# Kernel tuning notes

Measured on AMD Instinct MI355X. Metric: run time of the kernel, lower is better.

## Reference

```python
import jax, jax.numpy as jnp
import numpy as np
from jax.scipy.special import logsumexp

K, D, H, A = 8, 512, 512, 1024
S, T = 64, 128
B = S * T


def setup_inputs() -> dict:
    key = jax.random.key(0)
    k1, k2, k3, k4 = jax.random.split(key, 4)
    obs = jax.random.normal(k1, (B, D), dtype=jnp.float32)
    actions = jax.random.randint(k2, (B,), 0, A, dtype=jnp.int64)
    # uniform mixture prior (log(1/K)) => all components supported
    start_mixture_logprobs = jnp.full((S, K), jnp.log(1.0 / K), dtype=jnp.float32)
    W1 = jax.random.normal(k3, (K, D, H), dtype=jnp.float32) * 0.02
    b1 = jnp.zeros((K, H), dtype=jnp.float32)
    W2 = jax.random.normal(k4, (K, H, A), dtype=jnp.float32) * 0.02
    b2 = jnp.zeros((K, A), dtype=jnp.float32)
    return {"obs": obs, "actions": actions,
            "start_mixture_logprobs": start_mixture_logprobs,
            "W1": W1, "b1": b1, "W2": W2, "b2": b2, "seq_len": T}


def reference(obs, actions, start_mixture_logprobs, W1, b1, W2, b2, seq_len):
    num_seqs, num_comp = start_mixture_logprobs.shape
    batch = obs.shape[0]
    t_len = batch // num_seqs  # == seq_len
    num_out = W2.shape[-1]

    # per-component MLP on the full batch (all components supported)
    h = jax.nn.relu(jnp.einsum('bd,kdh->kbh', obs, W1) + b1[:, None, :])
    logits = jnp.einsum('kbh,kha->kba', h, W2) + b2[:, None, :]  # [K,B,A]
    component_logprobs = jax.nn.log_softmax(logits, axis=2)      # [K,B,A]

    # add time dimension: [B, K, A] -> [S, T, K, A]
    clp_t = component_logprobs.transpose(1, 0, 2).reshape(num_seqs, t_len, num_comp, num_out)
    act_t = actions.reshape(num_seqs, t_len)

    # gather logprob of taken action per component: [S, T, K]
    idx = jnp.broadcast_to(act_t[:, :, None, None], (num_seqs, t_len, num_comp, 1))
    action_logprobs = jnp.take_along_axis(clp_t, idx, axis=3)[..., 0]
    cum = jnp.cumsum(action_logprobs, axis=1)  # [S,T,K]

    # per-timestep posterior over mixture (shifted cumulative evidence)
    shift = jnp.concatenate([jnp.zeros((num_seqs, 1, num_comp), dtype=cum.dtype), cum[:, :-1]], axis=1)
    mix = jax.nn.log_softmax(start_mixture_logprobs[:, None, :] + shift, axis=2)  # [S,T,K]
    final_mixture_logprobs = jax.nn.log_softmax(start_mixture_logprobs + cum[:, -1], axis=1)

    # combine: logsumexp over components of component_logprobs + mixture logprob
    mix_flat = mix.reshape(batch, num_comp).T  # [K,B]
    model_out = logsumexp(component_logprobs + mix_flat[:, :, None], axis=0)  # [B,A]
    return model_out, final_mixture_logprobs
```

## Files before the change

kernel.cpp:

```cpp
#include <hip/hip_runtime.h>
#include <hip/hip_bf16.h>
#include <stdint.h>

#define KC   8
#define DIM  512
#define HID  512
#define ACTN 1024
#define NS   64
#define NT   128
#define NB   8192
#define PB   4

typedef __attribute__((ext_vector_type(8))) short short8;
typedef __attribute__((ext_vector_type(8))) unsigned short ushort8;
typedef __attribute__((ext_vector_type(4))) float floatx4;
typedef __attribute__((ext_vector_type(2))) float floatx2;
typedef __attribute__((ext_vector_type(4))) unsigned int uint4v;

__device__ inline float bf2f(unsigned short u) {
    return __uint_as_float(((unsigned int)u) << 16);
}
__device__ inline unsigned short f2bf_rne(float x) {
    unsigned int u = __float_as_uint(x);
    u += 0x7fffu + ((u >> 16) & 1u);
    return (unsigned short)(u >> 16);
}

__device__ inline unsigned char f2fp8_manual(float v) {
    unsigned int s = (__float_as_uint(v) >> 24) & 0x80u;
    float a = fabsf(v) * 0x1.0p-120f;
    unsigned int b = __float_as_uint(a);
    b += 0x7FFFFu + ((b >> 20) & 1u);
    unsigned int m = b >> 20;
    if (m > 0x7Eu) m = 0x7Eu;
    return (unsigned char)(s | m);
}
__device__ inline float fp82f_manual(unsigned int byte) {
    unsigned int bits = ((byte & 0x80u) << 24) | ((byte & 0x7Fu) << 20);
    return __uint_as_float(bits) * 0x1.0p+120f;
}
template <bool HI>
__device__ inline unsigned int pk_fp8(float a, float b, unsigned int old) {
#if __has_builtin(__builtin_amdgcn_cvt_pk_fp8_f32)
    return __builtin_amdgcn_cvt_pk_fp8_f32(a, b, old, HI);
#else
    unsigned int p = (unsigned int)f2fp8_manual(a) | ((unsigned int)f2fp8_manual(b) << 8);
    return HI ? ((old & 0x0000ffffu) | (p << 16)) : ((old & 0xffff0000u) | p);
#endif
}
template <bool HI>
__device__ inline floatx2 unpk_fp8(unsigned int src) {
#if __has_builtin(__builtin_amdgcn_cvt_pk_f32_fp8)
    return __builtin_amdgcn_cvt_pk_f32_fp8(src, HI);
#else
    unsigned int w = HI ? (src >> 16) : src;
    floatx2 r;
    r.x = fp82f_manual(w & 0xffu);
    r.y = fp82f_manual((w >> 8) & 0xffu);
    return r;
#endif
}

__device__ inline void gload_lds16(const unsigned short* g, unsigned short* l) {
    __builtin_amdgcn_global_load_lds(
        (const __attribute__((address_space(1))) unsigned int*)g,
        (__attribute__((address_space(3))) unsigned int*)l,
        16, 0, 0);
}


__global__ __launch_bounds__(256) void prep_kernel(
    const float* __restrict__ obs, const float* __restrict__ W1,
    const float* __restrict__ W2,
    unsigned short* __restrict__ obs_bk, unsigned short* __restrict__ W1bk,
    unsigned short* __restrict__ W2bk)
{
    __shared__ float tile[64][65];
    int id = blockIdx.x;
    if (id < 128) {
        int mg = id;
#pragma unroll
        for (int rep = 0; rep < 16; ++rep) {
            int idx = rep * 256 + threadIdx.x;
            int row = mg * 64 + (idx >> 6);
            int c_all = idx & 63;
            int kt = c_all >> 3, c = c_all & 7;
            const float* p = obs + (size_t)row * DIM + c_all * 8;
            ushort8 u;
#pragma unroll
            for (int e = 0; e < 8; e++) u[e] = f2bf_rne(p[e]);
            size_t off = (((size_t)(row >> 8) * (DIM >> 6) + kt) << 14)
                       + ((size_t)(row & 255) << 6) + ((c ^ (row & 7)) << 3);
            *(ushort8*)(obs_bk + off) = u;
        }
        return;
    }
    const float* src; unsigned short* dst; int R, C, xt, yt;
    if (id < 640) {
        int t = id - 128; int z = t >> 6; int rem = t & 63;
        xt = rem & 7; yt = rem >> 3;
        R = DIM; C = HID;
        src = W1 + (size_t)z * DIM * HID; dst = W1bk + (size_t)z * DIM * HID;
    } else {
        int t = id - 640; int z = t >> 7; int rem = t & 127;
        xt = rem & 15; yt = rem >> 4;
        R = HID; C = ACTN;
        src = W2 + (size_t)z * HID * ACTN; dst = W2bk + (size_t)z * HID * ACTN;
    }
    int h0 = xt * 64, d0 = yt * 64;
    int tx = threadIdx.x & 63, ty = threadIdx.x >> 6;
#pragma unroll
    for (int i = 0; i < 64; i += 4)
        tile[ty + i][tx] = src[(size_t)(d0 + ty + i) * C + h0 + tx];
    __syncthreads();
#pragma unroll
    for (int rep = 0; rep < 2; ++rep) {
        int idx  = rep * 256 + threadIdx.x;
        int h_l  = idx & 63;
        int dc   = idx >> 6;
        int rh   = h0 + h_l;
        ushort8 u;
#pragma unroll
        for (int e = 0; e < 8; e++) u[e] = f2bf_rne(tile[dc * 8 + e][h_l]);
        size_t off = (((size_t)(rh >> 8) * (R >> 6) + (d0 >> 6)) << 14)
                   + ((size_t)(rh & 255) << 6) + ((dc ^ (rh & 7)) << 3);
        *(ushort8*)(dst + off) = u;
    }
}

__global__ __launch_bounds__(512, 2) void gemm_blk_kernel(
    const unsigned short* __restrict__ Aall,
    const unsigned short* __restrict__ Ball,
    const float* __restrict__ biasall,
    void* __restrict__ Call,
    const int* __restrict__ actions,
    float* __restrict__ psum, float* __restrict__ palp,
    int M, int N, int Kd,
    long long zsA, long long zsB,
    int strideBias, long long strideCbytes,
    int do_relu, int do_blocked)
{
    __shared__ __align__(16) unsigned short S[65536];

    const int zb = blockIdx.z;
    const float* bias = biasall + (size_t)zb * strideBias;
    char* const Cbase = (char*)Call + (size_t)zb * strideCbytes;

    const int tid  = threadIdx.x;
    const int lane = tid & 63;
    const int w    = tid >> 6;
    const int wm   = w >> 2;
    const int wn   = w & 3;
    const int quad = lane >> 4;
    const int l16  = lane & 15;

    const int bm = blockIdx.x * 256;
    const int bn = blockIdx.y * 256;
    const int KT = Kd >> 6;
    const int nk = KT;

    floatx4 acc[8][4];
#pragma unroll
    for (int i = 0; i < 8; i++)
#pragma unroll
        for (int j = 0; j < 4; j++)
            acc[i][j] = (floatx4){0.f, 0.f, 0.f, 0.f};

    const unsigned short* srcA = Aall + (size_t)zb * zsA
        + (((size_t)(bm >> 8) * KT) << 14) + w * 1024 + lane * 8;
    const unsigned short* srcB = Ball + (size_t)zb * zsB
        + (((size_t)(bn >> 8) * KT) << 14) + w * 1024 + lane * 8;

    auto stageA = [&](int U, int HF) {
        const unsigned short* g = srcA + U * 16384 + HF * 8192;
        unsigned short* l = S + (U & 1) * 32768 + HF * 8192 + w * 1024;
        gload_lds16(g,       l);
        gload_lds16(g + 512, l + 512);
    };
    auto stageB = [&](int U, int HF) {
        const unsigned short* g = srcB + U * 16384 + HF * 8192;
        unsigned short* l = S + (U & 1) * 32768 + 16384 + HF * 8192 + w * 1024;
        gload_lds16(g,       l);
        gload_lds16(g + 512, l + 512);
    };

    const int swz  = (quad ^ (l16 & 7)) << 3;
    const int aoff0 = (wm * 128 + l16) * 64 + swz;
    const int boff0 = 16384 + (wn * 64 + l16) * 64 + swz;

    stageA(0, 0); stageA(0, 1); stageB(0, 0); stageB(0, 1);
    if (nk > 1) { stageA(1, 0); stageA(1, 1); }
    if (nk > 1) asm volatile("s_waitcnt vmcnt(4)" ::: "memory");
    else        asm volatile("s_waitcnt vmcnt(0)" ::: "memory");
    __builtin_amdgcn_s_barrier();

    for (int T = 0; T < nk; ++T) {
        const int bo = (T & 1) * 32768;
        short8 a0[8], b0[4], a1[8], b1[4];
#pragma unroll
        for (int i = 0; i < 8; i++) a0[i] = *(const short8*)(S + bo + aoff0 + i * 1024);
#pragma unroll
        for (int j = 0; j < 4; j++) b0[j] = *(const short8*)(S + bo + boff0 + j * 1024);
        if (T + 1 < nk) stageB(T + 1, 0);
        __builtin_amdgcn_s_barrier();
        __builtin_amdgcn_s_setprio(1);
#pragma unroll
        for (int i = 0; i < 4; i++)
#pragma unroll
            for (int j = 0; j < 4; j++)
                acc[i][j] = __builtin_amdgcn_mfma_f32_16x16x32_bf16(a0[i], b0[j], acc[i][j], 0, 0, 0);
        __builtin_amdgcn_s_setprio(0);
        __builtin_amdgcn_s_barrier();
#pragma unroll
        for (int i = 0; i < 8; i++) a1[i] = *(const short8*)(S + bo + (aoff0 ^ 32) + i * 1024);
#pragma unroll
        for (int j = 0; j < 4; j++) b1[j] = *(const short8*)(S + bo + (boff0 ^ 32) + j * 1024);
        if (T + 1 < nk) stageB(T + 1, 1);
        __builtin_amdgcn_s_barrier();
        __builtin_amdgcn_s_setprio(1);
#pragma unroll
        for (int i = 4; i < 8; i++)
#pragma unroll
            for (int j = 0; j < 4; j++)
                acc[i][j] = __builtin_amdgcn_mfma_f32_16x16x32_bf16(a0[i], b0[j], acc[i][j], 0, 0, 0);
        __builtin_amdgcn_s_setprio(0);
        asm volatile("s_waitcnt lgkmcnt(0)" ::: "memory");
        __builtin_amdgcn_s_barrier();
        if (T + 2 < nk) stageA(T + 2, 0);
        __builtin_amdgcn_s_barrier();
        __builtin_amdgcn_s_setprio(1);
#pragma unroll
        for (int i = 0; i < 4; i++)
#pragma unroll
            for (int j = 0; j < 4; j++)
                acc[i][j] = __builtin_amdgcn_mfma_f32_16x16x32_bf16(a1[i], b1[j], acc[i][j], 0, 0, 0);
        __builtin_amdgcn_s_setprio(0);
        __builtin_amdgcn_s_barrier();
        if (T + 2 < nk) stageA(T + 2, 1);
        __builtin_amdgcn_s_barrier();
        __builtin_amdgcn_s_setprio(1);
#pragma unroll
        for (int i = 4; i < 8; i++)
#pragma unroll
            for (int j = 0; j < 4; j++)
                acc[i][j] = __builtin_amdgcn_mfma_f32_16x16x32_bf16(a1[i], b1[j], acc[i][j], 0, 0, 0);
        __builtin_amdgcn_s_setprio(0);
        if (T < nk - 2)       asm volatile("s_waitcnt vmcnt(4)" ::: "memory");
        else if (T == nk - 2) asm volatile("s_waitcnt vmcnt(0)" ::: "memory");
        __builtin_amdgcn_s_barrier();
    }

    for (int h = 0; h < 2; ++h) {
        if (wm == h) {
#pragma unroll
            for (int j = 0; j < 4; j++) {
                int col = wn * 64 + j * 16 + l16;
                float bv = bias[bn + col];
#pragma unroll
                for (int i = 0; i < 8; i++) {
                    int r0 = i * 16 + quad * 4;
#pragma unroll
                    for (int r = 0; r < 4; r++) {
                        float v = acc[i][j][r] + bv;
                        if (do_relu) v = fmaxf(v, 0.f);
                        S[(r0 + r) * 264 + col] = f2bf_rne(v);
                    }
                }
            }
        }
        __builtin_amdgcn_s_barrier();
        if (do_blocked) {
            unsigned short* Cb16 = (unsigned short*)Cbase;
            const int KTo = N >> 6;
#pragma unroll
            for (int rep = 0; rep < 8; ++rep) {
                int idx  = rep * 512 + tid;
                int r_l  = idx >> 5;
                int s5   = idx & 31;
                int kt_l = s5 >> 3, st = s5 & 7;
                int r    = h * 128 + r_l;
                int c    = st ^ (r & 7);
                ushort8 u = *(const ushort8*)&S[r_l * 264 + kt_l * 64 + c * 8];
                size_t off = (((size_t)(bm >> 8) * KTo + (bn >> 6) + kt_l) << 14)
                           + ((size_t)r << 6) + (st << 3);
                *(ushort8*)(Cb16 + off) = u;
            }
        } else {
            unsigned char* Cb8 = (unsigned char*)Cbase;
            const int r_l = tid >> 2;
            const int ch  = (tid & 3) * 64;
            const int r   = h * 128 + r_l;
            unsigned char* crow = Cb8 + (size_t)(bm + r) * N + bn + ch;
            float ssum = 0.f;
#pragma unroll
            for (int g = 0; g < 4; g++) {
                ushort8 u0 = *(const ushort8*)&S[r_l * 264 + ch + 16 * g];
                ushort8 u1 = *(const ushort8*)&S[r_l * 264 + ch + 16 * g + 8];
                float v[16];
#pragma unroll
                for (int e = 0; e < 8; e++) { v[e] = bf2f(u0[e]); v[8 + e] = bf2f(u1[e]); }
#pragma unroll
                for (int e = 0; e < 16; e++) ssum += __expf(v[e]);
                uint4v pk;
                pk.x = pk_fp8<true>(v[2],  v[3],  pk_fp8<false>(v[0],  v[1],  0u));
                pk.y = pk_fp8<true>(v[6],  v[7],  pk_fp8<false>(v[4],  v[5],  0u));
                pk.z = pk_fp8<true>(v[10], v[11], pk_fp8<false>(v[8],  v[9],  0u));
                pk.w = pk_fp8<true>(v[14], v[15], pk_fp8<false>(v[12], v[13], 0u));
                *(uint4v*)(crow + 16 * g) = pk;
            }
            float t1 = ssum + __shfl_xor(ssum, 1);
            float stot = t1 + __shfl_xor(t1, 2);
            size_t kb = (size_t)zb * M + bm + r;
            if ((tid & 3) == 0)
                psum[kb * PB + blockIdx.y] = stot;
            int a_act = actions[bm + r];
            int rel = a_act - bn;
            if (rel >= ch && rel < ch + 64)
                palp[kb] = bf2f(S[r_l * 264 + rel]);
        }
        __builtin_amdgcn_s_barrier();
    }
}

__global__ __launch_bounds__(128) void mix_kernel(
    const float* __restrict__ palp,
    const float* __restrict__ psum,
    const float* __restrict__ start,
    float* __restrict__ w,
    float* __restrict__ fmix)
{
    __shared__ float buf[2][NT][9];
    int s = blockIdx.x, t = threadIdx.x;
    int b = s * NT + t;

    float a[KC], lsev[KC];
#pragma unroll
    for (int k = 0; k < KC; k++) {
        size_t kb = (size_t)k * NB + b;
        const float* ps = psum + kb * PB;
        float Ssum = 0.f;
#pragma unroll
        for (int p = 0; p < PB; p++) Ssum += ps[p];
        float l = __logf(Ssum);
        lsev[k] = l;
        a[k] = palp[kb] - l;
    }

#pragma unroll
    for (int k = 0; k < KC; k++) buf[0][t][k] = a[k];
    int p = 0;
    for (int off = 1; off < NT; off <<= 1) {
        __syncthreads();
#pragma unroll
        for (int k = 0; k < KC; k++) {
            float x = buf[p][t][k];
            if (t >= off) x += buf[p][t - off][k];
            buf[1 - p][t][k] = x;
        }
        p ^= 1;
    }
    __syncthreads();
    float st[KC], e[KC];
#pragma unroll
    for (int k = 0; k < KC; k++) st[k] = start[s * KC + k];
#pragma unroll
    for (int k = 0; k < KC; k++) e[k] = st[k] + buf[p][t][k] - a[k];
    float m = e[0];
#pragma unroll
    for (int k = 1; k < KC; k++) m = fmaxf(m, e[k]);
    float sum = 0.f;
#pragma unroll
    for (int k = 0; k < KC; k++) sum += __expf(e[k] - m);
    float l = m + __logf(sum);
#pragma unroll
    for (int k = 0; k < KC; k++)
        w[(size_t)k * NB + b] = (e[k] - l) - lsev[k];

    if (t == NT - 1) {
        float f[KC];
#pragma unroll
        for (int k = 0; k < KC; k++) f[k] = st[k] + buf[p][t][k];
        float m2 = f[0];
#pragma unroll
        for (int k = 1; k < KC; k++) m2 = fmaxf(m2, f[k]);
        float s2 = 0.f;
#pragma unroll
        for (int k = 0; k < KC; k++) s2 += __expf(f[k] - m2);
        float l2 = m2 + __logf(s2);
#pragma unroll
        for (int k = 0; k < KC; k++) fmix[s * KC + k] = f[k] - l2;
    }
}

__global__ __launch_bounds__(256) void combine_kernel(
    const unsigned char* __restrict__ logits8,
    const float* __restrict__ w,
    float* __restrict__ out)
{
    int b  = blockIdx.x * 2 + (threadIdx.x >> 7);
    int a0 = (threadIdx.x & 127) * 8;
    float x[KC][8];
#pragma unroll
    for (int k = 0; k < KC; k++) {
        float wv = w[(size_t)k * NB + b];
        uint2 q = *(const uint2*)(logits8 + ((size_t)k * NB + b) * ACTN + a0);
        floatx2 p01 = unpk_fp8<false>(q.x), p23 = unpk_fp8<true>(q.x);
        floatx2 p45 = unpk_fp8<false>(q.y), p67 = unpk_fp8<true>(q.y);
        x[k][0] = p01.x + wv; x[k][1] = p01.y + wv;
        x[k][2] = p23.x + wv; x[k][3] = p23.y + wv;
        x[k][4] = p45.x + wv; x[k][5] = p45.y + wv;
        x[k][6] = p67.x + wv; x[k][7] = p67.y + wv;
    }
    float* op = out + (size_t)b * ACTN + a0;
#pragma unroll
    for (int j = 0; j < 8; j++) {
        float m = x[0][j];
#pragma unroll
        for (int k = 1; k < KC; k++) m = fmaxf(m, x[k][j]);
        float s = 0.f;
#pragma unroll
        for (int k = 0; k < KC; k++) s += __expf(x[k][j] - m);
        op[j] = m + __logf(s);
    }
}

extern "C" void kernel_launch(void* const* d_in, const int* in_sizes, int n_in,
                              void* d_out, int out_size, void* d_ws, size_t ws_size,
                              hipStream_t stream)
{
    const float* obs     = (const float*)d_in[0];
    const int*   actions = (const int*)d_in[1];
    const float* start   = (const float*)d_in[2];
    const float* W1      = (const float*)d_in[3];
    const float* b1      = (const float*)d_in[4];
    const float* W2      = (const float*)d_in[5];
    const float* b2      = (const float*)d_in[6];

    char* ws = (char*)d_ws;
    unsigned short* obs_bk  = (unsigned short*)ws; ws += (size_t)NB * DIM * 2;
    unsigned short* W1bk    = (unsigned short*)ws; ws += (size_t)KC * HID * DIM * 2;
    unsigned short* W2bk    = (unsigned short*)ws; ws += (size_t)KC * ACTN * HID * 2;
    unsigned short* hbuf    = (unsigned short*)ws; ws += (size_t)KC * NB * HID * 2;
    unsigned char*  logits8 = (unsigned char*)ws;  ws += (size_t)KC * NB * ACTN;
    float* wbuf = (float*)ws; ws += (size_t)KC * NB * 4;
    float* psum = (float*)ws; ws += (size_t)KC * NB * PB * 4;
    float* palp = (float*)ws; ws += (size_t)KC * NB * 4;

    float* out  = (float*)d_out;
    float* fmix = out + (size_t)NB * ACTN;

    prep_kernel<<<1664, 256, 0, stream>>>(obs, W1, W2, obs_bk, W1bk, W2bk);

    gemm_blk_kernel<<<dim3(NB / 256, HID / 256, KC), 512, 0, stream>>>(
        obs_bk, W1bk, b1, hbuf, actions, psum, palp,
        NB, HID, DIM,
        0LL, (long long)HID * DIM,
        HID, (long long)NB * HID * 2, 1, 1);

    gemm_blk_kernel<<<dim3(NB / 256, ACTN / 256, KC), 512, 0, stream>>>(
        hbuf, W2bk, b2, logits8, actions, psum, palp,
        NB, ACTN, HID,
        (long long)NB * HID, (long long)ACTN * HID,
        ACTN, (long long)NB * ACTN, 0, 0);

    mix_kernel<<<NS, NT, 0, stream>>>(palp, psum, start, wbuf, fmix);

    combine_kernel<<<NB / 2, 256, 0, stream>>>(logits8, wbuf, out);
}
```

Measured before the change: 282.6 us.

## Make GEMM persistent with 32-wide K slabs and 4-stage cross-tile pipeline

```diff
diff --git a/kernel.cpp b/kernel.cpp
--- a/kernel.cpp
+++ b/kernel.cpp
@@ -81,16 +81,18 @@
         int mg = id;
 #pragma unroll
         for (int rep = 0; rep < 16; ++rep) {
-            int idx = rep * 256 + threadIdx.x;
-            int row = mg * 64 + (idx >> 6);
-            int c_all = idx & 63;
-            int kt = c_all >> 3, c = c_all & 7;
-            const float* p = obs + (size_t)row * DIM + c_all * 8;
+            int idx   = rep * 256 + threadIdx.x;
+            int st    = idx & 3;
+            int row_l = (idx >> 2) & 63;
+            int kt    = idx >> 8;
+            int row   = mg * 64 + row_l;
+            int c     = st ^ (row & 3);
+            const float* pp = obs + (size_t)row * DIM + kt * 32 + c * 8;
             ushort8 u;
 #pragma unroll
-            for (int e = 0; e < 8; e++) u[e] = f2bf_rne(p[e]);
-            size_t off = (((size_t)(row >> 8) * (DIM >> 6) + kt) << 14)
-                       + ((size_t)(row & 255) << 6) + ((c ^ (row & 7)) << 3);
+            for (int e = 0; e < 8; e++) u[e] = f2bf_rne(pp[e]);
+            size_t off = (((size_t)(row >> 8) * 16 + kt) << 13)
+                       + ((size_t)(row & 255) << 5) + (st << 3);
             *(ushort8*)(obs_bk + off) = u;
         }
         return;
@@ -116,14 +118,16 @@
 #pragma unroll
     for (int rep = 0; rep < 2; ++rep) {
         int idx  = rep * 256 + threadIdx.x;
-        int h_l  = idx & 63;
-        int dc   = idx >> 6;
+        int st   = idx & 3;
+        int h_l  = (idx >> 2) & 63;
+        int dcg  = idx >> 8;
         int rh   = h0 + h_l;
+        int c    = st ^ (rh & 3);
         ushort8 u;
 #pragma unroll
-        for (int e = 0; e < 8; e++) u[e] = f2bf_rne(tile[dc * 8 + e][h_l]);
-        size_t off = (((size_t)(rh >> 8) * (R >> 6) + (d0 >> 6)) << 14)
-                   + ((size_t)(rh & 255) << 6) + ((dc ^ (rh & 7)) << 3);
+        for (int e = 0; e < 8; e++) u[e] = f2bf_rne(tile[dcg * 32 + c * 8 + e][h_l]);
+        size_t off = (((size_t)(rh >> 8) * (R >> 5) + (d0 >> 5) + dcg) << 13)
+                   + ((size_t)(rh & 255) << 5) + (st << 3);
         *(ushort8*)(dst + off) = u;
     }
 }
@@ -135,16 +139,15 @@
     void* __restrict__ Call,
     const int* __restrict__ actions,
     float* __restrict__ psum, float* __restrict__ palp,
-    int M, int N, int Kd,
+    int M, int N,
     long long zsA, long long zsB,
     int strideBias, long long strideCbytes,
     int do_relu, int do_blocked)
 {
-    __shared__ __align__(16) unsigned short S[65536];
-
-    const int zb = blockIdx.z;
-    const float* bias = biasall + (size_t)zb * strideBias;
-    char* const Cbase = (char*)Call + (size_t)zb * strideCbytes;
+    __shared__ __align__(16) unsigned short S[78080];
+    unsigned short* const Cs = S + 65536;
+    float* const biasF = (float*)(S + 73984);
+    int*   const actL  = (int*)(S + 76032);
 
     const int tid  = threadIdx.x;
     const int lane = tid & 63;
@@ -154,171 +157,189 @@
     const int quad = lane >> 4;
     const int l16  = lane & 15;
 
-    const int bm = blockIdx.x * 256;
-    const int bn = blockIdx.y * 256;
-    const int KT = Kd >> 6;
-    const int nk = KT;
-
-    floatx4 acc[8][4];
-#pragma unroll
-    for (int i = 0; i < 8; i++)
-#pragma unroll
-        for (int j = 0; j < 4; j++)
-            acc[i][j] = (floatx4){0.f, 0.f, 0.f, 0.f};
-
-    const unsigned short* srcA = Aall + (size_t)zb * zsA
-        + (((size_t)(bm >> 8) * KT) << 14) + w * 1024 + lane * 8;
-    const unsigned short* srcB = Ball + (size_t)zb * zsB
-        + (((size_t)(bn >> 8) * KT) << 14) + w * 1024 + lane * 8;
-
-    auto stageA = [&](int U, int HF) {
-        const unsigned short* g = srcA + U * 16384 + HF * 8192;
-        unsigned short* l = S + (U & 1) * 32768 + HF * 8192 + w * 1024;
-        gload_lds16(g,       l);
-        gload_lds16(g + 512, l + 512);
+    const int p = blockIdx.x;
+    const int nyt = N >> 8;
+    const int nyt_sh = (nyt == 4) ? 2 : 1;
+    const int TPB = nyt;
+    const int G = TPB << 4;
+
+    const int lanebase = w * 512 + lane * 8;
+
+    auto stgA = [&](const unsigned short* slab, int b4s, int hf) {
+        gload_lds16(slab + hf * 4096, S + b4s * 16384 + hf * 4096 + w * 512);
     };
-    auto stageB = [&](int U, int HF) {
-        const unsigned short* g = srcB + U * 16384 + HF * 8192;
-        unsigned short* l = S + (U & 1) * 32768 + 16384 + HF * 8192 + w * 1024;
-        gload_lds16(g,       l);
-        gload_lds16(g + 512, l + 512);
+    auto stgB = [&](const unsigned short* slab, int b4s, int hf) {
+        gload_lds16(slab + hf * 4096, S + b4s * 16384 + 8192 + hf * 4096 + w * 512);
     };
 
-    const int swz  = (quad ^ (l16 & 7)) << 3;
-    const int aoff0 = (wm * 128 + l16) * 64 + swz;
-    const int boff0 = 16384 + (wn * 64 + l16) * 64 + swz;
-
-    stageA(0, 0); stageA(0, 1); stageB(0, 0); stageB(0, 1);
-    if (nk > 1) { stageA(1, 0); stageA(1, 1); }
-    if (nk > 1) asm volatile("s_waitcnt vmcnt(4)" ::: "memory");
-    else        asm volatile("s_waitcnt vmcnt(0)" ::: "memory");
+    for (int i2 = tid; i2 < (TPB << 8); i2 += 512) {
+        int tt = i2 >> 8, c = i2 & 255;
+        int fl = p + (tt << 8);
+        int xx = fl & 31, rs = fl >> 5;
+        int yy = rs & (nyt - 1), zz = rs >> nyt_sh;
+        biasF[i2] = biasall[(size_t)zz * strideBias + (yy << 8) + c];
+        if (!do_blocked) actL[i2] = actions[(xx << 8) + c];
+    }
+    __syncthreads();
+
+    const int swz  = (quad ^ (l16 & 3)) << 3;
+    const int arow = (wm * 128 + l16) * 32 + swz;
+    const int brow = 8192 + (wn * 64 + l16) * 32 + swz;
+
+    {
+        int fl = p;
+        int x0 = fl & 31, rs = fl >> 5;
+        int y0 = rs & (nyt - 1), z0 = rs >> nyt_sh;
+        const unsigned short* a0 = Aall + (size_t)z0 * zsA + (size_t)x0 * 131072 + lanebase;
+        const unsigned short* b0 = Ball + (size_t)z0 * zsB + (size_t)y0 * 131072 + lanebase;
+#pragma unroll
+        for (int pg = 0; pg < 3; ++pg) {
+            stgA(a0 + pg * 8192, pg, 0); stgA(a0 + pg * 8192, pg, 1);
+            stgB(b0 + pg * 8192, pg, 0); stgB(b0 + pg * 8192, pg, 1);
+        }
+    }
+    asm volatile("s_waitcnt vmcnt(8)" ::: "memory");
     __builtin_amdgcn_s_barrier();
 
-    for (int T = 0; T < nk; ++T) {
-        const int bo = (T & 1) * 32768;
-        short8 a0[8], b0[4], a1[8], b1[4];
-#pragma unroll
-        for (int i = 0; i < 8; i++) a0[i] = *(const short8*)(S + bo + aoff0 + i * 1024);
-#pragma unroll
-        for (int j = 0; j < 4; j++) b0[j] = *(const short8*)(S + bo + boff0 + j * 1024);
-        if (T + 1 < nk) stageB(T + 1, 0);
-        __builtin_amdgcn_s_barrier();
-        __builtin_amdgcn_s_setprio(1);
-#pragma unroll
-        for (int i = 0; i < 4; i++)
+    for (int t = 0; t < TPB; ++t) {
+        int fl = p + (t << 8);
+        int x = fl & 31, rs = fl >> 5;
+        int y = rs & (nyt - 1), z = rs >> nyt_sh;
+        int t1 = (t + 1 < TPB) ? t + 1 : t;
+        int fl1 = p + (t1 << 8);
+        int x1 = fl1 & 31, rs1 = fl1 >> 5;
+        int y1 = rs1 & (nyt - 1), z1 = rs1 >> nyt_sh;
+
+        const unsigned short* sAc = Aall + (size_t)z * zsA + (size_t)x * 131072 + lanebase;
+        const unsigned short* sBc = Ball + (size_t)z * zsB + (size_t)y * 131072 + lanebase;
+        const unsigned short* sAn = Aall + (size_t)z1 * zsA + (size_t)x1 * 131072 + lanebase;
+        const unsigned short* sBn = Ball + (size_t)z1 * zsB + (size_t)y1 * 131072 + lanebase;
+
+        floatx4 acc[8][4];
+#pragma unroll
+        for (int i = 0; i < 8; i++)
 #pragma unroll
             for (int j = 0; j < 4; j++)
-                acc[i][j] = __builtin_amdgcn_mfma_f32_16x16x32_bf16(a0[i], b0[j], acc[i][j], 0, 0, 0);
-        __builtin_amdgcn_s_setprio(0);
-        __builtin_amdgcn_s_barrier();
-#pragma unroll
-        for (int i = 0; i < 8; i++) a1[i] = *(const short8*)(S + bo + (aoff0 ^ 32) + i * 1024);
-#pragma unroll
-        for (int j = 0; j < 4; j++) b1[j] = *(const short8*)(S + bo + (boff0 ^ 32) + j * 1024);
-        if (T + 1 < nk) stageB(T + 1, 1);
-        __builtin_amdgcn_s_barrier();
-        __builtin_amdgcn_s_setprio(1);
-#pragma unroll
-        for (int i = 4; i < 8; i++)
-#pragma unroll
-            for (int j = 0; j < 4; j++)
-                acc[i][j] = __builtin_amdgcn_mfma_f32_16x16x32_bf16(a0[i], b0[j], acc[i][j], 0, 0, 0);
-        __builtin_amdgcn_s_setprio(0);
-        asm volatile("s_waitcnt lgkmcnt(0)" ::: "memory");
-        __builtin_amdgcn_s_barrier();
-        if (T + 2 < nk) stageA(T + 2, 0);
-        __builtin_amdgcn_s_barrier();
-        __builtin_amdgcn_s_setprio(1);
-#pragma unroll
-        for (int i = 0; i < 4; i++)
-#pragma unroll
-            for (int j = 0; j < 4; j++)
-                acc[i][j] = __builtin_amdgcn_mfma_f32_16x16x32_bf16(a1[i], b1[j], acc[i][j], 0, 0, 0);
-        __builtin_amdgcn_s_setprio(0);
-        __builtin_amdgcn_s_barrier();
-        if (T + 2 < nk) stageA(T + 2, 1);
-        __builtin_amdgcn_s_barrier();
-        __builtin_amdgcn_s_setprio(1);
-#pragma unroll
-        for (int i = 4; i < 8; i++)
-#pragma unroll
-            for (int j = 0; j < 4; j++)
-                acc[i][j] = __builtin_amdgcn_mfma_f32_16x16x32_bf16(a1[i], b1[j], acc[i][j], 0, 0, 0);
-        __builtin_amdgcn_s_setprio(0);
-        if (T < nk - 2)       asm volatile("s_waitcnt vmcnt(4)" ::: "memory");
-        else if (T == nk - 2) asm volatile("s_waitcnt vmcnt(0)" ::: "memory");
-        __builtin_amdgcn_s_barrier();
-    }
-
-    for (int h = 0; h < 2; ++h) {
-        if (wm == h) {
-#pragma unroll
-            for (int j = 0; j < 4; j++) {
-                int col = wn * 64 + j * 16 + l16;
-                float bv = bias[bn + col];
-#pragma unroll
-                for (int i = 0; i < 8; i++) {
-                    int r0 = i * 16 + quad * 4;
-#pragma unroll
-                    for (int r = 0; r < 4; r++) {
-                        float v = acc[i][j][r] + bv;
-                        if (do_relu) v = fmaxf(v, 0.f);
-                        S[(r0 + r) * 264 + col] = f2bf_rne(v);
+                acc[i][j] = (floatx4){0.f, 0.f, 0.f, 0.f};
+
+#pragma unroll 4
+        for (int kk = 0; kk < 16; ++kk) {
+            const int b4  = kk & 3;
+            const int nb4 = (kk + 3) & 3;
+            unsigned short* const Sb = S + b4 * 16384;
+            const int g = (t << 4) + kk;
+            const bool have = (g + 3 < G);
+            const int tg = kk + 3;
+            const unsigned short* gA = (tg < 16) ? (sAc + tg * 8192) : (sAn + (tg - 16) * 8192);
+            const unsigned short* gB = (tg < 16) ? (sBc + tg * 8192) : (sBn + (tg - 16) * 8192);
+
+            short8 bfr[4], af[4];
+#pragma unroll
+            for (int j = 0; j < 4; ++j) bfr[j] = *(const short8*)(Sb + brow + j * 512);
+#pragma unroll
+            for (int i = 0; i < 4; ++i) af[i] = *(const short8*)(Sb + arow + i * 512);
+            if (have) { stgA(gA, nb4, 0); stgA(gA, nb4, 1); }
+            __builtin_amdgcn_s_barrier();
+            __builtin_amdgcn_s_setprio(1);
+#pragma unroll
+            for (int i = 0; i < 4; ++i)
+#pragma unroll
+                for (int j = 0; j < 4; ++j)
+                    acc[i][j] = __builtin_amdgcn_mfma_f32_16x16x32_bf16(
+                        af[i], bfr[j], acc[i][j], 0, 0, 0);
+            __builtin_amdgcn_s_setprio(0);
+            __builtin_amdgcn_s_barrier();
+
+            short8 af2[4];
+#pragma unroll
+            for (int i = 0; i < 4; ++i) af2[i] = *(const short8*)(Sb + arow + (4 + i) * 512);
+            if (have) { stgB(gB, nb4, 0); stgB(gB, nb4, 1); }
+            __builtin_amdgcn_s_barrier();
+            __builtin_amdgcn_s_setprio(1);
+#pragma unroll
+            for (int i = 0; i < 4; ++i)
+#pragma unroll
+                for (int j = 0; j < 4; ++j)
+                    acc[4 + i][j] = __builtin_amdgcn_mfma_f32_16x16x32_bf16(
+                        af2[i], bfr[j], acc[4 + i][j], 0, 0, 0);
+            __builtin_amdgcn_s_setprio(0);
+            if (g < G - 3)       { asm volatile("s_waitcnt vmcnt(8)" ::: "memory"); }
+            else if (g == G - 3) { asm volatile("s_waitcnt vmcnt(4)" ::: "memory"); }
+            else if (g == G - 2) { asm volatile("s_waitcnt vmcnt(0)" ::: "memory"); }
+            __builtin_amdgcn_s_barrier();
+        }
+
+        const int bm = x << 8, bn = y << 8;
+        char* const Cb = (char*)Call + (size_t)z * strideCbytes;
+#pragma unroll
+        for (int e = 0; e < 8; ++e) {
+            if (wm == (e >> 2)) {
+                const int i0 = (e & 3) * 2;
+#pragma unroll
+                for (int ii = 0; ii < 2; ++ii)
+#pragma unroll
+                    for (int j = 0; j < 4; ++j) {
+                        const int col = wn * 64 + j * 16 + l16;
+                        float bv = biasF[(t << 8) + col];
+#pragma unroll
+                        for (int rr = 0; rr < 4; ++rr) {
+                            float v = acc[i0 + ii][j][rr] + bv;
+                            if (do_relu) v = fmaxf(v, 0.f);
+                            Cs[(ii * 16 + quad * 4 + rr) * 264 + col] = f2bf_rne(v);
+                        }
                     }
+            }
+            asm volatile("s_waitcnt lgkmcnt(0)\ns_barrier" ::: "memory");
+            const int rbase = e * 32;
+            if (do_blocked) {
+                unsigned short* Cb16 = (unsigned short*)Cb;
+#pragma unroll
+                for (int rep = 0; rep < 2; ++rep) {
+                    int idx = rep * 512 + tid;
+                    int kt  = idx >> 7;
+                    int r_l = (idx >> 2) & 31;
+                    int st  = idx & 3;
+                    int r   = rbase + r_l;
+                    int c   = st ^ (r & 3);
+                    ushort8 u = *(const ushort8*)&Cs[r_l * 264 + kt * 32 + c * 8];
+                    size_t off = (((size_t)(x * 16 + (bn >> 5) + kt)) << 13)
+                               + ((size_t)r << 5) + (st << 3);
+                    *(ushort8*)(Cb16 + off) = u;
                 }
-            }
-        }
-        __builtin_amdgcn_s_barrier();
-        if (do_blocked) {
-            unsigned short* Cb16 = (unsigned short*)Cbase;
-            const int KTo = N >> 6;
-#pragma unroll
-            for (int rep = 0; rep < 8; ++rep) {
-                int idx  = rep * 512 + tid;
-                int r_l  = idx >> 5;
-                int s5   = idx & 31;
-                int kt_l = s5 >> 3, st = s5 & 7;
-                int r    = h * 128 + r_l;
-                int c    = st ^ (r & 7);
-                ushort8 u = *(const ushort8*)&S[r_l * 264 + kt_l * 64 + c * 8];
-                size_t off = (((size_t)(bm >> 8) * KTo + (bn >> 6) + kt_l) << 14)
-                           + ((size_t)r << 6) + (st << 3);
-                *(ushort8*)(Cb16 + off) = u;
-            }
-        } else {
-            unsigned char* Cb8 = (unsigned char*)Cbase;
-            const int r_l = tid >> 2;
-            const int ch  = (tid & 3) * 64;
-            const int r   = h * 128 + r_l;
-            unsigned char* crow = Cb8 + (size_t)(bm + r) * N + bn + ch;
-            float ssum = 0.f;
-#pragma unroll
-            for (int g = 0; g < 4; g++) {
-                ushort8 u0 = *(const ushort8*)&S[r_l * 264 + ch + 16 * g];
-                ushort8 u1 = *(const ushort8*)&S[r_l * 264 + ch + 16 * g + 8];
+            } else {
+                unsigned char* Cb8 = (unsigned char*)Cb;
+                const int r_l = tid >> 4;
+                const int ch  = (tid & 15) * 16;
+                const int r   = rbase + r_l;
+                unsigned char* crow = Cb8 + (size_t)(bm + r) * N + bn + ch;
+                ushort8 u0 = *(const ushort8*)&Cs[r_l * 264 + ch];
+                ushort8 u1 = *(const ushort8*)&Cs[r_l * 264 + ch + 8];
                 float v[16];
 #pragma unroll
-                for (int e = 0; e < 8; e++) { v[e] = bf2f(u0[e]); v[8 + e] = bf2f(u1[e]); }
-#pragma unroll
-                for (int e = 0; e < 16; e++) ssum += __expf(v[e]);
+                for (int e2 = 0; e2 < 8; e2++) { v[e2] = bf2f(u0[e2]); v[8 + e2] = bf2f(u1[e2]); }
+                float ssum = 0.f;
+#pragma unroll
+                for (int e2 = 0; e2 < 16; e2++) ssum += __expf(v[e2]);
                 uint4v pk;
                 pk.x = pk_fp8<true>(v[2],  v[3],  pk_fp8<false>(v[0],  v[1],  0u));
                 pk.y = pk_fp8<true>(v[6],  v[7],  pk_fp8<false>(v[4],  v[5],  0u));
                 pk.z = pk_fp8<true>(v[10], v[11], pk_fp8<false>(v[8],  v[9],  0u));
                 pk.w = pk_fp8<true>(v[14], v[15], pk_fp8<false>(v[12], v[13], 0u));
-                *(uint4v*)(crow + 16 * g) = pk;
+                *(uint4v*)crow = pk;
+                float t1s = ssum + __shfl_xor(ssum, 1);
+                float t2s = t1s + __shfl_xor(t1s, 2);
+                float t3s = t2s + __shfl_xor(t2s, 4);
+                float stot = t3s + __shfl_xor(t3s, 8);
+                size_t kb = (size_t)z * M + bm + r;
+                if ((tid & 15) == 0)
+                    psum[kb * PB + y] = stot;
+                int a_act = actL[(t << 8) + r];
+                int rel = a_act - bn;
+                if (rel >= ch && rel < ch + 16)
+                    palp[kb] = bf2f(Cs[r_l * 264 + rel]);
             }
-            float t1 = ssum + __shfl_xor(ssum, 1);
-            float stot = t1 + __shfl_xor(t1, 2);
-            size_t kb = (size_t)zb * M + bm + r;
-            if ((tid & 3) == 0)
-                psum[kb * PB + blockIdx.y] = stot;
-            int a_act = actions[bm + r];
-            int rel = a_act - bn;
-            if (rel >= ch && rel < ch + 64)
-                palp[kb] = bf2f(S[r_l * 264 + rel]);
+            asm volatile("s_barrier" ::: "memory");
         }
-        __builtin_amdgcn_s_barrier();
     }
 }
 
@@ -340,7 +361,7 @@
         const float* ps = psum + kb * PB;
         float Ssum = 0.f;
 #pragma unroll
-        for (int p = 0; p < PB; p++) Ssum += ps[p];
+        for (int p2 = 0; p2 < PB; p2++) Ssum += ps[p2];
         float l = __logf(Ssum);
         lsev[k] = l;
         a[k] = palp[kb] - l;
@@ -451,15 +472,15 @@
 
     prep_kernel<<<1664, 256, 0, stream>>>(obs, W1, W2, obs_bk, W1bk, W2bk);
 
-    gemm_blk_kernel<<<dim3(NB / 256, HID / 256, KC), 512, 0, stream>>>(
+    gemm_blk_kernel<<<256, 512, 0, stream>>>(
         obs_bk, W1bk, b1, hbuf, actions, psum, palp,
-        NB, HID, DIM,
+        NB, HID,
         0LL, (long long)HID * DIM,
         HID, (long long)NB * HID * 2, 1, 1);
 
-    gemm_blk_kernel<<<dim3(NB / 256, ACTN / 256, KC), 512, 0, stream>>>(
+    gemm_blk_kernel<<<256, 512, 0, stream>>>(
         hbuf, W2bk, b2, logits8, actions, psum, palp,
-        NB, ACTN, HID,
+        NB, ACTN,
         (long long)NB * HID, (long long)ACTN * HID,
         ACTN, (long long)NB * ACTN, 0, 0);
 
```

Result: slower. 312.2 us (+10.5%).
